# Kernel tuning notes

Hardware: AMD Instinct MI355X
Metric: run time of the kernel (lower is better)

The kernel has to match this reference:

```python
import jax, jax.numpy as jnp
import numpy as np

HID = 256
POS_FREQ = 10
DIR_FREQ = 4
POS_ENC = 3 * (2 * POS_FREQ + 1)   # 63
DIR_ENC = 3 * (2 * DIR_FREQ + 1)   # 27
N_PTS = 262144


def _posenc(x, num_freq):
    freqs = (2.0 ** jnp.arange(num_freq)).astype(x.dtype)      # [F]
    xf = x[..., None, :] * freqs[:, None]                       # [..., F, D]
    sc = jnp.stack([jnp.sin(xf), jnp.cos(xf)], axis=-2)         # [..., F, 2, D]
    return jnp.concatenate([x, sc.reshape(*x.shape[:-1], -1)], axis=-1)


def _linear_init(key, fan_in, fan_out):
    kw, kb = jax.random.split(key)
    s = 1.0 / np.sqrt(fan_in)
    W = jax.random.uniform(kw, (fan_in, fan_out), jnp.float32, -s, s)
    b = jax.random.uniform(kb, (fan_out,), jnp.float32, -s, s)
    return W, b


def setup_inputs() -> dict:
    key = jax.random.key(0)
    ks = jax.random.split(key, 16)
    inp = {
        "positions": jax.random.normal(ks[0], (N_PTS, 3), jnp.float32),
        "directions": jax.random.normal(ks[1], (N_PTS, 3), jnp.float32),
    }
    W, b = _linear_init(ks[2], POS_ENC, HID)
    inp["W_in"], inp["b_in"] = W, b
    # 7 hidden layers; layer index 4 takes skip concat (HID + POS_ENC)
    for i in range(7):
        fan_in = HID + POS_ENC if i == 4 else HID
        W, b = _linear_init(ks[3 + i], fan_in, HID)
        inp[f"W_h{i}"], inp[f"b_h{i}"] = W, b
    W, b = _linear_init(ks[10], HID, HID + 1)
    inp["W_out"], inp["b_out"] = W, b
    W, b = _linear_init(ks[11], HID + DIR_ENC, HID // 2)
    inp["W_r1"], inp["b_r1"] = W, b
    W, b = _linear_init(ks[12], HID // 2, 3)
    inp["W_r2"], inp["b_r2"] = W, b
    return inp


def _forward(positions, directions, W_in, b_in, hidden_params, W_out, b_out,
             W_r1, b_r1, W_r2, b_r2):
    pe = _posenc(positions, POS_FREQ)    # [N, 63]
    de = _posenc(directions, DIR_FREQ)   # [N, 27]
    h = jax.nn.relu(pe @ W_in + b_in)    # [N, 256]
    for i, (W, b) in enumerate(hidden_params):
        if i == 4:
            h = jnp.concatenate([h, pe], axis=-1)  # skip connection [N, 319]
        h = jax.nn.relu(h @ W + b)
    out = h @ W_out + b_out                      # [N, 257]
    features = out[..., :HID]                    # [N, 256]
    density = jax.nn.relu(out[..., HID:HID + 1])  # [N, 1]
    rgb_in = jnp.concatenate([features, de], axis=-1)  # [N, 283]
    rgb = jax.nn.sigmoid(jax.nn.relu(rgb_in @ W_r1 + b_r1) @ W_r2 + b_r2)  # [N, 3]
    return rgb, density


def reference(positions, directions, W_in, b_in,
              W_h0, b_h0, W_h1, b_h1, W_h2, b_h2, W_h3, b_h3,
              W_h4, b_h4, W_h5, b_h5, W_h6, b_h6,
              W_out, b_out, W_r1, b_r1, W_r2, b_r2):
    hidden = [(W_h0, b_h0), (W_h1, b_h1), (W_h2, b_h2), (W_h3, b_h3),
              (W_h4, b_h4), (W_h5, b_h5), (W_h6, b_h6)]
    return _forward(positions, directions, W_in, b_in, hidden,
                    W_out, b_out, W_r1, b_r1, W_r2, b_r2)
```

## Files before the change

### kernel.cpp

```cpp
#include <hip/hip_runtime.h>
#include <math.h>

#define NPTS 262144
#define MT 64
#define XS 328

typedef __attribute__((ext_vector_type(8))) short bf16x8;
typedef __attribute__((ext_vector_type(4))) float f32x4;
typedef __attribute__((ext_vector_type(2))) unsigned int u32x2;

#if defined(__has_builtin)
#if __has_builtin(__builtin_amdgcn_cvt_pk_bf16_f32)
#define HAVE_CVT_PK_BF16 1
#endif
#endif

__device__ __forceinline__ short f2bf(float f) {
    union { float f; unsigned u; } v; v.f = f;
    unsigned r = v.u + 0x7fffu + ((v.u >> 16) & 1u);
    return (short)(r >> 16);
}
__device__ __forceinline__ unsigned pk2(float a, float b) {
#ifdef HAVE_CVT_PK_BF16
    auto r = __builtin_amdgcn_cvt_pk_bf16_f32(a, b);
    unsigned u; __builtin_memcpy(&u, &r, 4);
    return u;
#else
    return ((unsigned)(unsigned short)f2bf(a)) |
           ((unsigned)(unsigned short)f2bf(b) << 16);
#endif
}

#define OFF_IN   0
#define SZ_IN    (64*256)
#define OFF_H0   (OFF_IN + SZ_IN)
#define SZ_H     (256*256)
#define OFF_H1   (OFF_H0 + SZ_H)
#define OFF_H2   (OFF_H1 + SZ_H)
#define OFF_H3   (OFF_H2 + SZ_H)
#define OFF_H4   (OFF_H3 + SZ_H)
#define SZ_H4    (320*256)
#define OFF_H5   (OFF_H4 + SZ_H4)
#define OFF_H6   (OFF_H5 + SZ_H)
#define OFF_OUT  (OFF_H6 + SZ_H)
#define SZ_OUT   (256*272)
#define OFF_R1   (OFF_OUT + SZ_OUT)
#define SZ_R1    (288*128)
#define OFF_R2   (OFF_R1 + SZ_R1)
#define SZ_R2    (128*16)
#define WS_TOTAL (OFF_R2 + SZ_R2)

struct PrepP { const float* W[11]; short* ws; };

__global__ __launch_bounds__(256) void prep_all(PrepP pp) {
    int i = blockIdx.x * 256 + threadIdx.x;
    if (i >= WS_TOTAL) return;
    const int offs[12] = {OFF_IN, OFF_H0, OFF_H1, OFF_H2, OFF_H3, OFF_H4,
                          OFF_H5, OFF_H6, OFF_OUT, OFF_R1, OFF_R2, WS_TOTAL};
    const int Ks[11]  = {63,256,256,256,256,319,256,256,256,283,128};
    const int Ns[11]  = {256,256,256,256,256,256,256,256,257,128,3};
    const int Nps[11] = {256,256,256,256,256,256,256,256,272,128,16};
    int seg = 0;
    while (i >= offs[seg + 1]) seg++;
    int li = i - offs[seg];
    int j = li & 7, L = (li >> 3) & 63, tile = li >> 9;
    int nNt = Nps[seg] >> 4;
    int nt = tile % nNt, kt = tile / nNt;
    int k = kt * 32 + ((L >> 4) << 3) + j;
    int n = nt * 16 + (L & 15);
    float v = (k < Ks[seg] && n < Ns[seg]) ? pp.W[seg][k * Ns[seg] + n] : 0.f;
    pp.ws[i] = f2bf(v);
}

struct Params {
    const float *pos, *dir;
    const float *b_in, *b_h0, *b_h1, *b_h2, *b_h3, *b_h4, *b_h5, *b_h6;
    const float *b_out, *b_r1, *b_r2;
    const short *w;
    float *out;
};

template<int NKT, int NT, int NS, int TM, int MODE>
__device__ __forceinline__ void layerT(const short* __restrict__ Wsw,
                                       const float* __restrict__ bias,
                                       short* X, float* dout, int p0,
                                       int ntB, int mtB, int wave, int lane) {
    const int l15 = lane & 15, quad = lane >> 4;
    __syncthreads();
    const short* xb = X + l15 * XS + quad * 8;

    if (MODE == 1) {
        f32x4 ad = (f32x4){0.f, 0.f, 0.f, 0.f};
        for (int kt = 0; kt < NKT; ++kt) {
            bf16x8 b = *(const bf16x8*)(xb + wave * 16 * XS + kt * 32);
            bf16x8 a = *(const bf16x8*)(Wsw + (size_t)((kt * NT + 16) * 64 + lane) * 8);
            ad = __builtin_amdgcn_mfma_f32_16x16x32_bf16(a, b, ad, 0, 0, 0);
        }
        if (quad == 0)
            dout[3 * NPTS + p0 + wave * 16 + l15] = fmaxf(ad[0] + bias[256], 0.f);
    }

    f32x4 acc[NS][TM];
#pragma unroll
    for (int s = 0; s < NS; s++)
#pragma unroll
        for (int t = 0; t < TM; t++) acc[s][t] = (f32x4){0.f, 0.f, 0.f, 0.f};

    const short* wp = Wsw + (size_t)((ntB)*64 + lane) * 8;

    bf16x8 a_c[NS], b_c[TM];
#pragma unroll
    for (int s = 0; s < NS; s++)
        a_c[s] = *(const bf16x8*)(wp + (size_t)s * 512);
#pragma unroll
    for (int t = 0; t < TM; t++)
        b_c[t] = *(const bf16x8*)(xb + (mtB + t) * 16 * XS);

#pragma unroll
    for (int kt = 0; kt < NKT; ++kt) {
        bf16x8 a_n[NS], b_n[TM];
        if (kt + 1 < NKT) {
            const short* wp1 = wp + (size_t)(kt + 1) * NT * 512;
#pragma unroll
            for (int s = 0; s < NS; s++)
                a_n[s] = *(const bf16x8*)(wp1 + (size_t)s * 512);
#pragma unroll
            for (int t = 0; t < TM; t++)
                b_n[t] = *(const bf16x8*)(xb + (mtB + t) * 16 * XS + (kt + 1) * 32);
        }
#pragma unroll
        for (int s = 0; s < NS; s++)
#pragma unroll
            for (int t = 0; t < TM; t++)
                acc[s][t] = __builtin_amdgcn_mfma_f32_16x16x32_bf16(a_c[s], b_c[t], acc[s][t], 0, 0, 0);
        if (kt + 1 < NKT) {
#pragma unroll
            for (int s = 0; s < NS; s++) a_c[s] = a_n[s];
#pragma unroll
            for (int t = 0; t < TM; t++) b_c[t] = b_n[t];
        }
    }
    __syncthreads();
#pragma unroll
    for (int s = 0; s < NS; s++) {
        const int n0 = (ntB + s) * 16 + quad * 4;
        const f32x4 bv = *(const f32x4*)(bias + n0);
#pragma unroll
        for (int t = 0; t < TM; t++) {
            const int m = (mtB + t) * 16 + l15;
            float v0 = acc[s][t][0] + bv[0];
            float v1 = acc[s][t][1] + bv[1];
            float v2 = acc[s][t][2] + bv[2];
            float v3 = acc[s][t][3] + bv[3];
            if (MODE == 0) {
                v0 = fmaxf(v0, 0.f); v1 = fmaxf(v1, 0.f);
                v2 = fmaxf(v2, 0.f); v3 = fmaxf(v3, 0.f);
            }
            u32x2 w; w[0] = pk2(v0, v1); w[1] = pk2(v2, v3);
            *(u32x2*)(X + m * XS + n0) = w;
        }
    }
}

__global__ __launch_bounds__(256, 3) void nerf_fused(Params P) {
    __shared__ __align__(16) short X[MT * XS];
    __shared__ __align__(16) short DE[MT * 32];
    const int tid = threadIdx.x;
    const int wave = tid >> 6, lane = tid & 63;
    const int p0 = blockIdx.x * MT;

    const int ntB_h = wave * 4;
    const int ntB_r = wave * 2;

    for (int i = tid; i < MT * 64; i += 256) {
        const int pt = i >> 6, d = i & 63;
        float v = 0.f;
        if (d < 3) v = P.pos[(p0 + pt) * 3 + d];
        else if (d < 63) {
            const int e = d - 3, f = e / 6, r = e % 6;
            const float x = P.pos[(p0 + pt) * 3 + (r % 3)];
            const float xf = x * (float)(1 << f);
            v = (r < 3) ? sinf(xf) : cosf(xf);
        }
        const short bv = f2bf(v);
        X[pt * XS + d] = bv;
        X[pt * XS + 256 + d] = bv;
    }
    for (int i = tid; i < MT * 32; i += 256) {
        const int pt = i >> 5, d = i & 31;
        float v = 0.f;
        if (d < 3) v = P.dir[(p0 + pt) * 3 + d];
        else if (d < 27) {
            const int e = d - 3, f = e / 6, r = e % 6;
            const float x = P.dir[(p0 + pt) * 3 + (r % 3)];
            const float xf = x * (float)(1 << f);
            v = (r < 3) ? sinf(xf) : cosf(xf);
        }
        DE[i] = f2bf(v);
    }

    layerT<2, 16, 4, 4, 0>(P.w + OFF_IN, P.b_in, X, P.out, p0, ntB_h, 0, wave, lane);
    layerT<8, 16, 4, 4, 0>(P.w + OFF_H0, P.b_h0, X, P.out, p0, ntB_h, 0, wave, lane);
    layerT<8, 16, 4, 4, 0>(P.w + OFF_H1, P.b_h1, X, P.out, p0, ntB_h, 0, wave, lane);
    layerT<8, 16, 4, 4, 0>(P.w + OFF_H2, P.b_h2, X, P.out, p0, ntB_h, 0, wave, lane);
    layerT<8, 16, 4, 4, 0>(P.w + OFF_H3, P.b_h3, X, P.out, p0, ntB_h, 0, wave, lane);
    layerT<10, 16, 4, 4, 0>(P.w + OFF_H4, P.b_h4, X, P.out, p0, ntB_h, 0, wave, lane);
    layerT<8, 16, 4, 4, 0>(P.w + OFF_H5, P.b_h5, X, P.out, p0, ntB_h, 0, wave, lane);
    layerT<8, 16, 4, 4, 0>(P.w + OFF_H6, P.b_h6, X, P.out, p0, ntB_h, 0, wave, lane);
    layerT<8, 17, 4, 4, 1>(P.w + OFF_OUT, P.b_out, X, P.out, p0, ntB_h, 0, wave, lane);

    for (int i = tid; i < MT * 32; i += 256) {
        const int pt = i >> 5, d = i & 31;
        X[pt * XS + 256 + d] = DE[i];
    }

    layerT<9, 8, 2, 4, 0>(P.w + OFF_R1, P.b_r1, X, P.out, p0, ntB_r, 0, wave, lane);

    __syncthreads();
    {
        const int l15 = lane & 15, quad = lane >> 4;
        f32x4 acc = (f32x4){0.f, 0.f, 0.f, 0.f};
        const short* xb = X + (wave * 16 + l15) * XS + quad * 8;
#pragma unroll
        for (int kt = 0; kt < 4; ++kt) {
            bf16x8 b = *(const bf16x8*)(xb + kt * 32);
            bf16x8 a = *(const bf16x8*)(P.w + OFF_R2 + (size_t)(kt * 64 + lane) * 8);
            acc = __builtin_amdgcn_mfma_f32_16x16x32_bf16(a, b, acc, 0, 0, 0);
        }
        if (quad == 0) {
#pragma unroll
            for (int r = 0; r < 3; r++) {
                const float v = acc[r] + P.b_r2[r];
                P.out[(size_t)(p0 + wave * 16 + l15) * 3 + r] = 1.f / (1.f + expf(-v));
            }
        }
    }
}

extern "C" void kernel_launch(void* const* d_in, const int* in_sizes, int n_in,
                              void* d_out, int out_size, void* d_ws, size_t ws_size,
                              hipStream_t stream) {
    short* ws = (short*)d_ws;

    PrepP pp;
    pp.W[0]  = (const float*)d_in[2];
    pp.W[1]  = (const float*)d_in[4];
    pp.W[2]  = (const float*)d_in[6];
    pp.W[3]  = (const float*)d_in[8];
    pp.W[4]  = (const float*)d_in[10];
    pp.W[5]  = (const float*)d_in[12];
    pp.W[6]  = (const float*)d_in[14];
    pp.W[7]  = (const float*)d_in[16];
    pp.W[8]  = (const float*)d_in[18];
    pp.W[9]  = (const float*)d_in[20];
    pp.W[10] = (const float*)d_in[22];
    pp.ws = ws;
    hipLaunchKernelGGL(prep_all, dim3((WS_TOTAL + 255) / 256), dim3(256), 0, stream, pp);

    Params P;
    P.pos  = (const float*)d_in[0];
    P.dir  = (const float*)d_in[1];
    P.b_in = (const float*)d_in[3];
    P.b_h0 = (const float*)d_in[5];
    P.b_h1 = (const float*)d_in[7];
    P.b_h2 = (const float*)d_in[9];
    P.b_h3 = (const float*)d_in[11];
    P.b_h4 = (const float*)d_in[13];
    P.b_h5 = (const float*)d_in[15];
    P.b_h6 = (const float*)d_in[17];
    P.b_out = (const float*)d_in[19];
    P.b_r1 = (const float*)d_in[21];
    P.b_r2 = (const float*)d_in[23];
    P.w = ws;
    P.out = (float*)d_out;
    hipLaunchKernelGGL(nerf_fused, dim3(NPTS / MT), dim3(256), 0, stream, P);
}
```

Baseline: 428.5 us.

## Recompute positional encoding in registers to shrink LDS tile and raise occupancy

Removes the stored positional-encoding columns from the shared activation tile, cutting its row stride from 328 to 264 shorts. The input layer and the skip layer now build the encoding fragments in registers with sin/cos right before their MFMAs. The rgb layer reads the direction encoding from its own LDS buffer instead of copying it into X. The smaller LDS footprint allows launch bounds to ask for 4 blocks per CU instead of 3. The cost is recomputing sin/cos twice per point and extra register pressure under the tighter occupancy target.

Result: slower. 1.022 ms (+138.5%).

```diff
diff --git a/kernel.cpp b/kernel.cpp
--- a/kernel.cpp
+++ b/kernel.cpp
@@ -3,7 +3,7 @@
 
 #define NPTS 262144
 #define MT 64
-#define XS 328
+#define XS 264
 
 typedef __attribute__((ext_vector_type(8))) short bf16x8;
 typedef __attribute__((ext_vector_type(4))) float f32x4;
@@ -29,6 +29,28 @@
     return ((unsigned)(unsigned short)f2bf(a)) |
            ((unsigned)(unsigned short)f2bf(b) << 16);
 #endif
+}
+
+__device__ __forceinline__ bf16x8 pe_frag(float x0, float x1, float x2, int base) {
+    float vv[8];
+#pragma unroll
+    for (int j = 0; j < 8; j++) {
+        const int d = base + j;
+        float v = 0.f;
+        if (d < 3) v = (d == 0) ? x0 : ((d == 1) ? x1 : x2);
+        else if (d < 63) {
+            const int e = d - 3, f = e / 6, r = e % 6;
+            const int c = (r < 3) ? r : r - 3;
+            const float x = (c == 0) ? x0 : ((c == 1) ? x1 : x2);
+            const float xf = x * (float)(1 << f);
+            v = (r < 3) ? sinf(xf) : cosf(xf);
+        }
+        vv[j] = v;
+    }
+    union { unsigned u4[4]; bf16x8 b; } cv;
+    cv.u4[0] = pk2(vv[0], vv[1]); cv.u4[1] = pk2(vv[2], vv[3]);
+    cv.u4[2] = pk2(vv[4], vv[5]); cv.u4[3] = pk2(vv[6], vv[7]);
+    return cv.b;
 }
 
 #define OFF_IN   0
@@ -80,14 +102,30 @@
     float *out;
 };
 
-template<int NKT, int NT, int NS, int TM, int MODE>
+template<int NKT, int NT, int NS, int TM, int MODE, int PEKT, int DEKT>
 __device__ __forceinline__ void layerT(const short* __restrict__ Wsw,
                                        const float* __restrict__ bias,
-                                       short* X, float* dout, int p0,
-                                       int ntB, int mtB, int wave, int lane) {
+                                       short* X, const short* DE,
+                                       const float* __restrict__ pos,
+                                       float* dout, int p0,
+                                       int ntB, int wave, int lane) {
     const int l15 = lane & 15, quad = lane >> 4;
+    constexpr int NKTL = NKT - PEKT - DEKT;
+    const short* xb = X + l15 * XS + quad * 8;
+    const short* wp = Wsw + (size_t)(ntB * 64 + lane) * 8;
+
+    float px[TM], py[TM], pz[TM];
+    if (PEKT > 0) {
+#pragma unroll
+        for (int t = 0; t < TM; t++) {
+            const int pt = p0 + t * 16 + l15;
+            px[t] = pos[pt * 3 + 0];
+            py[t] = pos[pt * 3 + 1];
+            pz[t] = pos[pt * 3 + 2];
+        }
+    }
+
     __syncthreads();
-    const short* xb = X + l15 * XS + quad * 8;
 
     if (MODE == 1) {
         f32x4 ad = (f32x4){0.f, 0.f, 0.f, 0.f};
@@ -106,40 +144,72 @@
 #pragma unroll
         for (int t = 0; t < TM; t++) acc[s][t] = (f32x4){0.f, 0.f, 0.f, 0.f};
 
-    const short* wp = Wsw + (size_t)((ntB)*64 + lane) * 8;
-
-    bf16x8 a_c[NS], b_c[TM];
-#pragma unroll
-    for (int s = 0; s < NS; s++)
-        a_c[s] = *(const bf16x8*)(wp + (size_t)s * 512);
-#pragma unroll
-    for (int t = 0; t < TM; t++)
-        b_c[t] = *(const bf16x8*)(xb + (mtB + t) * 16 * XS);
-
-#pragma unroll
-    for (int kt = 0; kt < NKT; ++kt) {
-        bf16x8 a_n[NS], b_n[TM];
-        if (kt + 1 < NKT) {
-            const short* wp1 = wp + (size_t)(kt + 1) * NT * 512;
+    if (NKTL > 0) {
+        bf16x8 a_c[NS], b_c[TM];
+#pragma unroll
+        for (int s = 0; s < NS; s++)
+            a_c[s] = *(const bf16x8*)(wp + (size_t)s * 512);
+#pragma unroll
+        for (int t = 0; t < TM; t++)
+            b_c[t] = *(const bf16x8*)(xb + t * 16 * XS);
+
+#pragma unroll
+        for (int kt = 0; kt < NKTL; ++kt) {
+            bf16x8 a_n[NS], b_n[TM];
+            if (kt + 1 < NKTL) {
+                const short* wp1 = wp + (size_t)(kt + 1) * NT * 512;
+#pragma unroll
+                for (int s = 0; s < NS; s++)
+                    a_n[s] = *(const bf16x8*)(wp1 + (size_t)s * 512);
+#pragma unroll
+                for (int t = 0; t < TM; t++)
+                    b_n[t] = *(const bf16x8*)(xb + t * 16 * XS + (kt + 1) * 32);
+            }
 #pragma unroll
             for (int s = 0; s < NS; s++)
-                a_n[s] = *(const bf16x8*)(wp1 + (size_t)s * 512);
-#pragma unroll
-            for (int t = 0; t < TM; t++)
-                b_n[t] = *(const bf16x8*)(xb + (mtB + t) * 16 * XS + (kt + 1) * 32);
-        }
+#pragma unroll
+                for (int t = 0; t < TM; t++)
+                    acc[s][t] = __builtin_amdgcn_mfma_f32_16x16x32_bf16(a_c[s], b_c[t], acc[s][t], 0, 0, 0);
+            if (kt + 1 < NKTL) {
+#pragma unroll
+                for (int s = 0; s < NS; s++) a_c[s] = a_n[s];
+#pragma unroll
+                for (int t = 0; t < TM; t++) b_c[t] = b_n[t];
+            }
+        }
+    }
+
+#pragma unroll
+    for (int w = 0; w < PEKT; w++) {
+        const int kt = NKTL + w;
+        bf16x8 a[NS];
 #pragma unroll
         for (int s = 0; s < NS; s++)
-#pragma unroll
-            for (int t = 0; t < TM; t++)
-                acc[s][t] = __builtin_amdgcn_mfma_f32_16x16x32_bf16(a_c[s], b_c[t], acc[s][t], 0, 0, 0);
-        if (kt + 1 < NKT) {
-#pragma unroll
-            for (int s = 0; s < NS; s++) a_c[s] = a_n[s];
-#pragma unroll
-            for (int t = 0; t < TM; t++) b_c[t] = b_n[t];
-        }
-    }
+            a[s] = *(const bf16x8*)(wp + (size_t)kt * NT * 512 + (size_t)s * 512);
+#pragma unroll
+        for (int t = 0; t < TM; t++) {
+            bf16x8 b = pe_frag(px[t], py[t], pz[t], w * 32 + quad * 8);
+#pragma unroll
+            for (int s = 0; s < NS; s++)
+                acc[s][t] = __builtin_amdgcn_mfma_f32_16x16x32_bf16(a[s], b, acc[s][t], 0, 0, 0);
+        }
+    }
+
+    if (DEKT > 0) {
+        const int kt = NKT - 1;
+        bf16x8 a[NS];
+#pragma unroll
+        for (int s = 0; s < NS; s++)
+            a[s] = *(const bf16x8*)(wp + (size_t)kt * NT * 512 + (size_t)s * 512);
+#pragma unroll
+        for (int t = 0; t < TM; t++) {
+            bf16x8 b = *(const bf16x8*)(DE + (t * 16 + l15) * 32 + quad * 8);
+#pragma unroll
+            for (int s = 0; s < NS; s++)
+                acc[s][t] = __builtin_amdgcn_mfma_f32_16x16x32_bf16(a[s], b, acc[s][t], 0, 0, 0);
+        }
+    }
+
     __syncthreads();
 #pragma unroll
     for (int s = 0; s < NS; s++) {
@@ -147,7 +217,7 @@
         const f32x4 bv = *(const f32x4*)(bias + n0);
 #pragma unroll
         for (int t = 0; t < TM; t++) {
-            const int m = (mtB + t) * 16 + l15;
+            const int m = t * 16 + l15;
             float v0 = acc[s][t][0] + bv[0];
             float v1 = acc[s][t][1] + bv[1];
             float v2 = acc[s][t][2] + bv[2];
@@ -162,7 +232,7 @@
     }
 }
 
-__global__ __launch_bounds__(256, 3) void nerf_fused(Params P) {
+__global__ __launch_bounds__(256, 4) void nerf_fused(Params P) {
     __shared__ __align__(16) short X[MT * XS];
     __shared__ __align__(16) short DE[MT * 32];
     const int tid = threadIdx.x;
@@ -172,20 +242,6 @@
     const int ntB_h = wave * 4;
     const int ntB_r = wave * 2;
 
-    for (int i = tid; i < MT * 64; i += 256) {
-        const int pt = i >> 6, d = i & 63;
-        float v = 0.f;
-        if (d < 3) v = P.pos[(p0 + pt) * 3 + d];
-        else if (d < 63) {
-            const int e = d - 3, f = e / 6, r = e % 6;
-            const float x = P.pos[(p0 + pt) * 3 + (r % 3)];
-            const float xf = x * (float)(1 << f);
-            v = (r < 3) ? sinf(xf) : cosf(xf);
-        }
-        const short bv = f2bf(v);
-        X[pt * XS + d] = bv;
-        X[pt * XS + 256 + d] = bv;
-    }
     for (int i = tid; i < MT * 32; i += 256) {
         const int pt = i >> 5, d = i & 31;
         float v = 0.f;
@@ -199,22 +255,16 @@
         DE[i] = f2bf(v);
     }
 
-    layerT<2, 16, 4, 4, 0>(P.w + OFF_IN, P.b_in, X, P.out, p0, ntB_h, 0, wave, lane);
-    layerT<8, 16, 4, 4, 0>(P.w + OFF_H0, P.b_h0, X, P.out, p0, ntB_h, 0, wave, lane);
-    layerT<8, 16, 4, 4, 0>(P.w + OFF_H1, P.b_h1, X, P.out, p0, ntB_h, 0, wave, lane);
-    layerT<8, 16, 4, 4, 0>(P.w + OFF_H2, P.b_h2, X, P.out, p0, ntB_h, 0, wave, lane);
-    layerT<8, 16, 4, 4, 0>(P.w + OFF_H3, P.b_h3, X, P.out, p0, ntB_h, 0, wave, lane);
-    layerT<10, 16, 4, 4, 0>(P.w + OFF_H4, P.b_h4, X, P.out, p0, ntB_h, 0, wave, lane);
-    layerT<8, 16, 4, 4, 0>(P.w + OFF_H5, P.b_h5, X, P.out, p0, ntB_h, 0, wave, lane);
-    layerT<8, 16, 4, 4, 0>(P.w + OFF_H6, P.b_h6, X, P.out, p0, ntB_h, 0, wave, lane);
-    layerT<8, 17, 4, 4, 1>(P.w + OFF_OUT, P.b_out, X, P.out, p0, ntB_h, 0, wave, lane);
-
-    for (int i = tid; i < MT * 32; i += 256) {
-        const int pt = i >> 5, d = i & 31;
-        X[pt * XS + 256 + d] = DE[i];
-    }
-
-    layerT<9, 8, 2, 4, 0>(P.w + OFF_R1, P.b_r1, X, P.out, p0, ntB_r, 0, wave, lane);
+    layerT<2, 16, 4, 4, 0, 2, 0>(P.w + OFF_IN, P.b_in, X, DE, P.pos, P.out, p0, ntB_h, wave, lane);
+    layerT<8, 16, 4, 4, 0, 0, 0>(P.w + OFF_H0, P.b_h0, X, DE, P.pos, P.out, p0, ntB_h, wave, lane);
+    layerT<8, 16, 4, 4, 0, 0, 0>(P.w + OFF_H1, P.b_h1, X, DE, P.pos, P.out, p0, ntB_h, wave, lane);
+    layerT<8, 16, 4, 4, 0, 0, 0>(P.w + OFF_H2, P.b_h2, X, DE, P.pos, P.out, p0, ntB_h, wave, lane);
+    layerT<8, 16, 4, 4, 0, 0, 0>(P.w + OFF_H3, P.b_h3, X, DE, P.pos, P.out, p0, ntB_h, wave, lane);
+    layerT<10, 16, 4, 4, 0, 2, 0>(P.w + OFF_H4, P.b_h4, X, DE, P.pos, P.out, p0, ntB_h, wave, lane);
+    layerT<8, 16, 4, 4, 0, 0, 0>(P.w + OFF_H5, P.b_h5, X, DE, P.pos, P.out, p0, ntB_h, wave, lane);
+    layerT<8, 16, 4, 4, 0, 0, 0>(P.w + OFF_H6, P.b_h6, X, DE, P.pos, P.out, p0, ntB_h, wave, lane);
+    layerT<8, 17, 4, 4, 1, 0, 0>(P.w + OFF_OUT, P.b_out, X, DE, P.pos, P.out, p0, ntB_h, wave, lane);
+    layerT<9, 8, 2, 4, 0, 0, 1>(P.w + OFF_R1, P.b_r1, X, DE, P.pos, P.out, p0, ntB_r, wave, lane);
 
     __syncthreads();
     {
```
